# Kernel tuning notes

Measured on AMD Instinct MI355X. Metric: run time of the kernel, lower is better.

## Reference

```python
import jax, jax.numpy as jnp
import numpy as np
from jax import lax

WBITS = 4
BN_EPS = 1e-5


def quantize_weight_symmetric(w, wbits=WBITS):
    # Per-tensor symmetric uniform quantization with straight-through estimator.
    qmax = float(2 ** (wbits - 1) - 1)  # 7 for 4-bit
    scale = jnp.max(jnp.abs(w)) / qmax
    wq = jnp.clip(jnp.round(w / scale), -qmax, qmax) * scale
    # STE: forward uses wq, backward passes gradient straight through to w
    return w + lax.stop_gradient(wq - w)


def setup_inputs() -> dict:
    key = jax.random.key(0)
    k1, k2 = jax.random.split(key)
    x = jax.random.normal(k1, (32, 128, 56, 56), dtype=jnp.float32)
    w = jax.random.normal(k2, (256, 128, 3, 3), dtype=jnp.float32) * 0.05
    gamma = jnp.ones((256,), dtype=jnp.float32)
    beta = jnp.zeros((256,), dtype=jnp.float32)
    return {"x": x, "w": w, "gamma": gamma, "beta": beta}


def reference(x, w, gamma, beta):
    # Quantized conv (QConv, bias=False, stride=1, padding=1)
    wq = quantize_weight_symmetric(w)
    out = lax.conv_general_dilated(
        x, wq,
        window_strides=(1, 1),
        padding=[(1, 1), (1, 1)],
        dimension_numbers=("NCHW", "OIHW", "NCHW"),
    )  # [N, 256, 56, 56]
    # BatchNorm2d in training mode: batch statistics over (N, H, W)
    mean = jnp.mean(out, axis=(0, 2, 3))
    var = jnp.var(out, axis=(0, 2, 3))
    inv = gamma * lax.rsqrt(var + BN_EPS)
    out = out * inv[None, :, None, None] + (beta - mean * inv)[None, :, None, None]
    # abits=32 -> full-precision activation (ReLU)
    return jax.nn.relu(out)
```

## Files before the change

kernel.cpp:

```cpp
#include <hip/hip_runtime.h>

typedef unsigned short u16;
typedef unsigned int u32;
typedef __attribute__((ext_vector_type(4))) float f32x4;
typedef __attribute__((ext_vector_type(8))) short short8;

#define HWD 56
#define HW2 3136
#define C_IN 128
#define K_OUT 256
#define N_IMG 32
#define CHW_IN 401408
#define CHW_OUT 802816
#define PIX 100352
#define WQ_N 294912
#define GROWS 1872
#define XROW 1856
#define XPLANE (GROWS * XROW)
#define NR 12
#define BCHUNKS 2784
#define NSLICE 1568
#define CV_OFF 33554432u
#define WS_NEED_BF16 (CV_OFF + (size_t)PIX * K_OUT * 2)

__device__ __forceinline__ u16 f2bf(float f) {
    u32 u = __float_as_uint(f);
    u32 r = u + 0x7FFFu + ((u >> 16) & 1u);
    return (u16)(r >> 16);
}

__device__ __forceinline__ void glds16(const u16* g, u16* l) {
    __builtin_amdgcn_global_load_lds(
        (const __attribute__((address_space(1))) void*)g,
        (__attribute__((address_space(3))) void*)l, 16, 0, 0);
}

__global__ void maxabs_k(const float* __restrict__ w, u32* __restrict__ wsmax) {
    float m = 0.f;
    for (int i = blockIdx.x * blockDim.x + threadIdx.x; i < WQ_N; i += gridDim.x * blockDim.x)
        m = fmaxf(m, fabsf(w[i]));
    for (int off = 32; off; off >>= 1)
        m = fmaxf(m, __shfl_xor(m, off));
    __shared__ float sm[4];
    int lane = threadIdx.x & 63, wid = threadIdx.x >> 6;
    if (lane == 0) sm[wid] = m;
    __syncthreads();
    if (threadIdx.x == 0) {
        float mm = fmaxf(fmaxf(sm[0], sm[1]), fmaxf(sm[2], sm[3]));
        atomicMax(wsmax, __float_as_uint(mm));
    }
}

__global__ void quant_t_k4(const float* __restrict__ w, const u32* __restrict__ wsmax,
                           u16* __restrict__ wqt4) {
    int o = blockIdx.x * 256 + threadIdx.x;
    if (o >= WQ_N) return;
    int j = o & 7;
    int m = (o >> 3) & 255;
    int oct = (o >> 11) & 3;
    int kt = o >> 13;
    int cq = kt / 9, tap = kt - cq * 9;
    int c = cq * 32 + oct * 8 + j;
    float scale = __uint_as_float(wsmax[0]) / 7.0f;
    float q = rintf(w[(m * 128 + c) * 9 + tap] / scale);
    q = fminf(fmaxf(q, -7.0f), 7.0f);
    wqt4[o] = f2bf(q * scale);
}

__global__ void halo_zero(u16* __restrict__ xt3) {
    int i = blockIdx.x * 256 + threadIdx.x;
    u32 addr;
    if (i < 74240) {
        int rowIdx = i / 928, rem = i - rowIdx * 928;
        int cq = rem / 232, c = rem - cq * 232;
        int row = rowIdx < 64 ? (rowIdx >> 1) * 58 + (rowIdx & 1) * 57 : 1856 + (rowIdx - 64);
        addr = (u32)cq * XPLANE + row * XROW + c * 8;
    } else {
        int j = i - 74240;
        int rowd = j >> 5, rem = j & 31;
        int side = rem >> 4, cq = (rem >> 2) & 3, o4 = rem & 3;
        int n = rowd / 56, h = rowd - n * 56;
        int row = n * 58 + 1 + h, col = side * 57;
        addr = (u32)cq * XPLANE + (row * 58 + col) * 32 + o4 * 8;
    }
    *(uint4*)(xt3 + addr) = (uint4){0, 0, 0, 0};
}

__global__ __launch_bounds__(256) void pad_transpose(const float* __restrict__ x,
                                                     u16* __restrict__ xt3) {
    __shared__ float T[128][57];
    const int tid = threadIdx.x;
    const int n = blockIdx.x / HWD;
    const int h = blockIdx.x - n * HWD;
    const float* srow = x + (size_t)n * CHW_IN + h * HWD;
    #pragma unroll
    for (int it = 0; it < 7; ++it) {
        int i = tid + it * 256;
        int c = i / 14, q = i - c * 14;
        float4 v = *(const float4*)(srow + c * HW2 + q * 4);
        T[c][q * 4 + 0] = v.x; T[c][q * 4 + 1] = v.y;
        T[c][q * 4 + 2] = v.z; T[c][q * 4 + 3] = v.w;
    }
    __syncthreads();
    const int gRow = n * 58 + 1 + h;
    #pragma unroll
    for (int it = 0; it < 4; ++it) {
        int i = tid + it * 256;
        if (i < 56 * 16) {
            int w = i >> 4, oc = i & 15;
            int cq = oc >> 2, o4 = oc & 3;
            union { u16 us[8]; uint4 v4; } pk;
            #pragma unroll
            for (int j = 0; j < 8; ++j) pk.us[j] = f2bf(T[oc * 8 + j][w]);
            *(uint4*)(xt3 + (size_t)cq * XPLANE + (gRow * 58 + (w + 1)) * 32 + o4 * 8) = pk.v4;
        }
    }
}

template <bool BF16OUT>
__global__ __launch_bounds__(512, 2) void conv_m(const u16* __restrict__ xt3,
                                                 const u16* __restrict__ wqt4,
                                                 float* __restrict__ out,
                                                 u16* __restrict__ cvout,
                                                 float* __restrict__ P) {
    __shared__ __align__(16) u16 lds[52416];
    const int tid = threadIdx.x;
    const int lane = tid & 63;
    const int w8 = tid >> 6;
    const int wm = w8 >> 2, wn = w8 & 3;
    const int fr = lane & 15, fq = lane >> 4;
    const int nt = (blockIdx.x & 7) * 49 + (blockIdx.x >> 3);
    const int p0 = nt * 256;
    const int R0 = (p0 / HW2) * 58 + (p0 % HW2) / HWD;

    int bElem[4];
    #pragma unroll
    for (int ni = 0; ni < 4; ++ni) {
        int px = p0 + wn * 64 + ni * 16 + fr;
        int img = px / HW2, hw = px - img * HW2;
        int gr = img * 58 + 1 + hw / HWD;
        int pixLin = (gr - R0) * 58 + (hw % HWD) + 1;
        bElem[ni] = (pixLin - 59) * 40 + fq * 8;
    }
    const int aBase = 27840 + fq * 2048 + (wm * 128 + fr) * 8;

#define GATE2() asm volatile("s_waitcnt vmcnt(2)" ::: "memory")
#define GATE0() asm volatile("s_waitcnt vmcnt(0)" ::: "memory")
#define BAR() __builtin_amdgcn_s_barrier()

    f32x4 acc[8][4];
    #pragma unroll
    for (int a = 0; a < 8; ++a)
        #pragma unroll
        for (int b = 0; b < 4; ++b)
            acc[a][b] = (f32x4){0.f, 0.f, 0.f, 0.f};

    #pragma unroll 1
    for (int cq = 0; cq < 4; ++cq) {
        {
            const u16* bsrc = xt3 + (size_t)cq * XPLANE + (size_t)R0 * XROW;
            uint4 breg[6];
            #pragma unroll
            for (int i = 0; i < 6; ++i) {
                int c = tid + i * 512;
                if (c < BCHUNKS) breg[i] = *(const uint4*)(bsrc + c * 8);
            }
            if (cq == 0) {
                glds16(wqt4 + tid * 8,              &lds[27840 + tid * 8]);
                glds16(wqt4 + (tid + 512) * 8,      &lds[27840 + (tid + 512) * 8]);
                glds16(wqt4 + 8192 + tid * 8,       &lds[27840 + 8192 + tid * 8]);
                glds16(wqt4 + 8192 + (tid + 512) * 8, &lds[27840 + 8192 + (tid + 512) * 8]);
            }
            #pragma unroll
            for (int i = 0; i < 6; ++i) {
                int c = tid + i * 512;
                if (c < BCHUNKS)
                    *(uint4*)&lds[(c >> 2) * 40 + (c & 3) * 8] = breg[i];
            }
        }
        __syncthreads();

        #pragma unroll
        for (int it = 0; it < 3; ++it) {
            #pragma unroll
            for (int u = 0; u < 3; ++u) {
                const int kt = cq * 9 + it * 3 + u;
                if (kt + 2 < 36) {
                    const u16* ga = wqt4 + (kt + 2) * 8192;
                    u16* da = &lds[27840 + ((u + 2) % 3) * 8192];
                    glds16(ga + tid * 8, da + tid * 8);
                    glds16(ga + (tid + 512) * 8, da + (tid + 512) * 8);
                }
                short8 pf[4], wf[4];
                #pragma unroll
                for (int ni = 0; ni < 4; ++ni)
                    pf[ni] = *(const short8*)&lds[bElem[ni] + it * 2320 + u * 40];
                #pragma unroll
                for (int mi = 0; mi < 4; ++mi)
                    wf[mi] = *(const short8*)&lds[aBase + u * 8192 + mi * 128];
                __builtin_amdgcn_s_setprio(1);
                #pragma unroll
                for (int mi = 0; mi < 4; ++mi)
                    #pragma unroll
                    for (int ni = 0; ni < 4; ++ni)
                        acc[mi][ni] = __builtin_amdgcn_mfma_f32_16x16x32_bf16(
                            pf[ni], wf[mi], acc[mi][ni], 0, 0, 0);
                __builtin_amdgcn_s_setprio(0);
                #pragma unroll
                for (int mi = 0; mi < 4; ++mi)
                    wf[mi] = *(const short8*)&lds[aBase + u * 8192 + (mi + 4) * 128];
                __builtin_amdgcn_s_setprio(1);
                #pragma unroll
                for (int mi = 0; mi < 4; ++mi)
                    #pragma unroll
                    for (int ni = 0; ni < 4; ++ni)
                        acc[mi + 4][ni] = __builtin_amdgcn_mfma_f32_16x16x32_bf16(
                            pf[ni], wf[mi], acc[mi + 4][ni], 0, 0, 0);
                __builtin_amdgcn_s_setprio(0);
                if (kt < 34) GATE2();
                else if (kt == 34) GATE0();
                BAR();
            }
        }
    }

    const int slice = nt * 4 + wn;
    #pragma unroll
    for (int mi = 0; mi < 8; ++mi) {
        float s = 0.f, q = 0.f;
        #pragma unroll
        for (int ni = 0; ni < 4; ++ni)
            #pragma unroll
            for (int j = 0; j < 4; ++j) {
                float v = acc[mi][ni][j];
                s += v; q += v * v;
            }
        s += __shfl_xor(s, 16); s += __shfl_xor(s, 32);
        q += __shfl_xor(q, 16); q += __shfl_xor(q, 32);
        if (fq == 0) {
            int ch = wm * 128 + mi * 16 + fr;
            float* dst = P + ((size_t)ch * NSLICE + slice) * 2;
            dst[0] = s; dst[1] = q;
        }
    }

    if (BF16OUT) {
        u16* T = lds;
        #pragma unroll
        for (int p = 0; p < 2; ++p) {
            __syncthreads();
            #pragma unroll
            for (int c2 = 0; c2 < 4; ++c2) {
                const int lch = wm * 64 + c2 * 16 + fr;
                #pragma unroll
                for (int ni = 0; ni < 4; ++ni) {
                    union { u16 h[4]; uint2 v; } pk;
                    #pragma unroll
                    for (int j = 0; j < 4; ++j) pk.h[j] = f2bf(acc[p * 4 + c2][ni][j]);
                    *(uint2*)&T[lch * 264 + wn * 64 + ni * 16 + fq * 4] = pk.v;
                }
            }
            __syncthreads();
            #pragma unroll
            for (int i = 0; i < 8; ++i) {
                int chunk = tid + i * 512;
                int lch = chunk >> 5, pxc = chunk & 31;
                uint4 v = *(const uint4*)&T[lch * 264 + pxc * 8];
                int ch = (lch >> 6) * 128 + p * 64 + (lch & 63);
                *(uint4*)&cvout[(size_t)ch * PIX + p0 + pxc * 8] = v;
            }
        }
    } else {
        #pragma unroll
        for (int mi = 0; mi < 8; ++mi) {
            int ch = wm * 128 + mi * 16 + fr;
            #pragma unroll
            for (int ni = 0; ni < 4; ++ni)
                #pragma unroll
                for (int j = 0; j < 4; ++j) {
                    int px = p0 + wn * 64 + ni * 16 + fq * 4 + j;
                    int n = px / HW2, hw = px - n * HW2;
                    out[(size_t)n * CHW_OUT + (size_t)ch * HW2 + hw] = acc[mi][ni][j];
                }
        }
    }
#undef GATE2
#undef GATE0
#undef BAR
}

__global__ void stats_fin(const float* __restrict__ P, const float* __restrict__ gamma,
                          const float* __restrict__ beta, float* __restrict__ stats) {
    int ch = blockIdx.x;
    int tid = threadIdx.x;
    float s = 0.f, q = 0.f;
    const float* base = P + (size_t)ch * NSLICE * 2;
    for (int i = tid; i < NSLICE; i += 256) {
        float2 v = *(const float2*)(base + i * 2);
        s += v.x; q += v.y;
    }
    for (int m = 32; m; m >>= 1) { s += __shfl_xor(s, m); q += __shfl_xor(q, m); }
    __shared__ float ss[4], qs[4];
    int l = tid & 63, w = tid >> 6;
    if (l == 0) { ss[w] = s; qs[w] = q; }
    __syncthreads();
    if (tid == 0) {
        float S = ss[0] + ss[1] + ss[2] + ss[3];
        float Q = qs[0] + qs[1] + qs[2] + qs[3];
        float mean = S / (float)PIX;
        float var = Q / (float)PIX - mean * mean;
        float inv = gamma[ch] * rsqrtf(var + 1e-5f);
        stats[2 * ch] = inv;
        stats[2 * ch + 1] = beta[ch] - mean * inv;
    }
}

__global__ void bn_relu_nchw(const u16* __restrict__ cvout, float* __restrict__ out,
                             const float* __restrict__ stats) {
    const int b = blockIdx.x;
    const int ch = b / 49, g = b - ch * 49;
    const float inv = stats[2 * ch], sh = stats[2 * ch + 1];
    const int p8 = (g * 256 + threadIdx.x) * 8;
    short8 v = *(const short8*)&cvout[(size_t)ch * PIX + p8];
    const int n = p8 / HW2;
    const int hw = p8 - n * HW2;
    float* dst = out + ((size_t)n * K_OUT + ch) * HW2 + hw;
    f32x4 o0, o1;
    #pragma unroll
    for (int j = 0; j < 4; ++j) {
        float a = __uint_as_float(((u32)(u16)v[j]) << 16);
        float bb = __uint_as_float(((u32)(u16)v[j + 4]) << 16);
        o0[j] = fmaxf(a * inv + sh, 0.f);
        o1[j] = fmaxf(bb * inv + sh, 0.f);
    }
    *(f32x4*)dst = o0;
    *(f32x4*)(dst + 4) = o1;
}

__global__ void bn_relu_f32(float* __restrict__ out, const float* __restrict__ stats) {
    const int n4 = ((size_t)N_IMG * K_OUT * HW2) / 4;
    int stride = gridDim.x * blockDim.x;
    for (int i = blockIdx.x * blockDim.x + threadIdx.x; i < n4; i += stride) {
        int ch = (i / (HW2 / 4)) & (K_OUT - 1);
        float inv = stats[2 * ch], sh = stats[2 * ch + 1];
        f32x4 v = ((f32x4*)out)[i];
        #pragma unroll
        for (int j = 0; j < 4; ++j)
            v[j] = fmaxf(v[j] * inv + sh, 0.f);
        ((f32x4*)out)[i] = v;
    }
}

extern "C" void kernel_launch(void* const* d_in, const int* in_sizes, int n_in,
                              void* d_out, int out_size, void* d_ws, size_t ws_size,
                              hipStream_t stream) {
    const float* x = (const float*)d_in[0];
    const float* w = (const float*)d_in[1];
    const float* gamma = (const float*)d_in[2];
    const float* beta = (const float*)d_in[3];
    float* out = (float*)d_out;

    char* ws = (char*)d_ws;
    u32* wsmax = (u32*)ws;
    float* stats = (float*)(ws + 64);
    u16* wqt4 = (u16*)(ws + 4096);
    float* P = (float*)(ws + 1048576u);
    u16* xt3 = (u16*)(ws + 4325376u);
    u16* cvout = (u16*)(ws + CV_OFF);
    const bool bf16path = (ws_size >= WS_NEED_BF16);

    hipMemsetAsync(wsmax, 0, 64, stream);
    maxabs_k<<<128, 256, 0, stream>>>(w, wsmax);
    quant_t_k4<<<WQ_N / 256, 256, 0, stream>>>(w, wsmax, wqt4);
    halo_zero<<<514, 256, 0, stream>>>(xt3);
    pad_transpose<<<N_IMG * HWD, 256, 0, stream>>>(x, xt3);
    if (bf16path) {
        conv_m<true><<<392, 512, 0, stream>>>(xt3, wqt4, out, cvout, P);
        stats_fin<<<K_OUT, 256, 0, stream>>>(P, gamma, beta, stats);
        bn_relu_nchw<<<K_OUT * 49, 256, 0, stream>>>(cvout, out, stats);
    } else {
        conv_m<false><<<392, 512, 0, stream>>>(xt3, wqt4, out, cvout, P);
        stats_fin<<<K_OUT, 256, 0, stream>>>(P, gamma, beta, stats);
        bn_relu_f32<<<4096, 256, 0, stream>>>(out, stats);
    }
}
```

Before: 150.3 us.

## Split conv output channels across two 256-thread blocks per pixel tile

Each 512-thread block used to compute all 256 output channels for a 256-pixel tile. Now 784 blocks of 256 threads each compute one 128-channel half, with the weight layout rearranged so each half is contiguous. The input tile in LDS is trimmed to 10 rows and weight staging starts before the loop. This shrinks LDS per block to allow more resident blocks and finer scheduling, at the cost of loading each input tile twice across the two halves.

```diff
diff --git a/kernel.cpp b/kernel.cpp
--- a/kernel.cpp
+++ b/kernel.cpp
@@ -17,8 +17,10 @@
 #define GROWS 1872
 #define XROW 1856
 #define XPLANE (GROWS * XROW)
-#define NR 12
-#define BCHUNKS 2784
+#define NR 10
+#define BCHUNKS 2320
+#define BPITCH 40
+#define BELEMS 23200
 #define NSLICE 1568
 #define CV_OFF 33554432u
 #define WS_NEED_BF16 (CV_OFF + (size_t)PIX * K_OUT * 2)
@@ -51,20 +53,22 @@
     }
 }
 
-__global__ void quant_t_k4(const float* __restrict__ w, const u32* __restrict__ wsmax,
-                           u16* __restrict__ wqt4) {
+__global__ void quant_t_k5(const float* __restrict__ w, const u32* __restrict__ wsmax,
+                           u16* __restrict__ wqt) {
     int o = blockIdx.x * 256 + threadIdx.x;
     if (o >= WQ_N) return;
     int j = o & 7;
-    int m = (o >> 3) & 255;
-    int oct = (o >> 11) & 3;
+    int mrow = (o >> 3) & 127;
+    int oct = (o >> 10) & 3;
+    int mt = (o >> 12) & 1;
     int kt = o >> 13;
     int cq = kt / 9, tap = kt - cq * 9;
     int c = cq * 32 + oct * 8 + j;
+    int m = mt * 128 + mrow;
     float scale = __uint_as_float(wsmax[0]) / 7.0f;
     float q = rintf(w[(m * 128 + c) * 9 + tap] / scale);
     q = fminf(fmaxf(q, -7.0f), 7.0f);
-    wqt4[o] = f2bf(q * scale);
+    wqt[o] = f2bf(q * scale);
 }
 
 __global__ void halo_zero(u16* __restrict__ xt3) {
@@ -118,32 +122,37 @@
 }
 
 template <bool BF16OUT>
-__global__ __launch_bounds__(512, 2) void conv_m(const u16* __restrict__ xt3,
-                                                 const u16* __restrict__ wqt4,
+__global__ __launch_bounds__(256, 2) void conv_m(const u16* __restrict__ xt3,
+                                                 const u16* __restrict__ wqt,
                                                  float* __restrict__ out,
                                                  u16* __restrict__ cvout,
                                                  float* __restrict__ P) {
-    __shared__ __align__(16) u16 lds[52416];
+    __shared__ __align__(16) u16 lds[35488];
     const int tid = threadIdx.x;
     const int lane = tid & 63;
-    const int w8 = tid >> 6;
-    const int wm = w8 >> 2, wn = w8 & 3;
+    const int w4 = tid >> 6;
     const int fr = lane & 15, fq = lane >> 4;
-    const int nt = (blockIdx.x & 7) * 49 + (blockIdx.x >> 3);
+    const int swz = (blockIdx.x & 7) * 98 + (blockIdx.x >> 3);
+    const int nt = swz >> 1, mt = swz & 1;
     const int p0 = nt * 256;
     const int R0 = (p0 / HW2) * 58 + (p0 % HW2) / HWD;
 
     int bElem[4];
     #pragma unroll
     for (int ni = 0; ni < 4; ++ni) {
-        int px = p0 + wn * 64 + ni * 16 + fr;
+        int px = p0 + w4 * 64 + ni * 16 + fr;
         int img = px / HW2, hw = px - img * HW2;
         int gr = img * 58 + 1 + hw / HWD;
         int pixLin = (gr - R0) * 58 + (hw % HWD) + 1;
-        bElem[ni] = (pixLin - 59) * 40 + fq * 8;
-    }
-    const int aBase = 27840 + fq * 2048 + (wm * 128 + fr) * 8;
-
+        bElem[ni] = (pixLin - 59) * BPITCH + fq * 8;
+    }
+
+#define ABUF(b) (&lds[BELEMS + (b) * 4096])
+#define STAGE_A(kt_, b_) do {                                              \
+        const u16* ga_ = wqt + (size_t)(((kt_) * 2 + mt)) * 4096;          \
+        glds16(ga_ + tid * 8,         ABUF(b_) + tid * 8);                 \
+        glds16(ga_ + (tid + 256) * 8, ABUF(b_) + (tid + 256) * 8);         \
+    } while (0)
 #define GATE2() asm volatile("s_waitcnt vmcnt(2)" ::: "memory")
 #define GATE0() asm volatile("s_waitcnt vmcnt(0)" ::: "memory")
 #define BAR() __builtin_amdgcn_s_barrier()
@@ -154,28 +163,26 @@
         #pragma unroll
         for (int b = 0; b < 4; ++b)
             acc[a][b] = (f32x4){0.f, 0.f, 0.f, 0.f};
+
+    STAGE_A(0, 0);
+    STAGE_A(1, 1);
 
     #pragma unroll 1
     for (int cq = 0; cq < 4; ++cq) {
         {
             const u16* bsrc = xt3 + (size_t)cq * XPLANE + (size_t)R0 * XROW;
-            uint4 breg[6];
-            #pragma unroll
-            for (int i = 0; i < 6; ++i) {
-                int c = tid + i * 512;
+            uint4 breg[10];
+            #pragma unroll
+            for (int i = 0; i < 10; ++i) {
+                int c = tid + i * 256;
                 if (c < BCHUNKS) breg[i] = *(const uint4*)(bsrc + c * 8);
             }
-            if (cq == 0) {
-                glds16(wqt4 + tid * 8,              &lds[27840 + tid * 8]);
-                glds16(wqt4 + (tid + 512) * 8,      &lds[27840 + (tid + 512) * 8]);
-                glds16(wqt4 + 8192 + tid * 8,       &lds[27840 + 8192 + tid * 8]);
-                glds16(wqt4 + 8192 + (tid + 512) * 8, &lds[27840 + 8192 + (tid + 512) * 8]);
-            }
-            #pragma unroll
-            for (int i = 0; i < 6; ++i) {
-                int c = tid + i * 512;
+            GATE0();
+            #pragma unroll
+            for (int i = 0; i < 10; ++i) {
+                int c = tid + i * 256;
                 if (c < BCHUNKS)
-                    *(uint4*)&lds[(c >> 2) * 40 + (c & 3) * 8] = breg[i];
+                    *(uint4*)&lds[(c >> 2) * BPITCH + (c & 3) * 8] = breg[i];
             }
         }
         __syncthreads();
@@ -184,20 +191,16 @@
         for (int it = 0; it < 3; ++it) {
             #pragma unroll
             for (int u = 0; u < 3; ++u) {
-                const int kt = cq * 9 + it * 3 + u;
-                if (kt + 2 < 36) {
-                    const u16* ga = wqt4 + (kt + 2) * 8192;
-                    u16* da = &lds[27840 + ((u + 2) % 3) * 8192];
-                    glds16(ga + tid * 8, da + tid * 8);
-                    glds16(ga + (tid + 512) * 8, da + (tid + 512) * 8);
-                }
+                const int tt = it * 3 + u;
+                const int kt = cq * 9 + tt;
+                if (kt + 2 < 36) STAGE_A(kt + 2, (tt + 2) % 3);
                 short8 pf[4], wf[4];
                 #pragma unroll
                 for (int ni = 0; ni < 4; ++ni)
-                    pf[ni] = *(const short8*)&lds[bElem[ni] + it * 2320 + u * 40];
+                    pf[ni] = *(const short8*)&lds[bElem[ni] + (it * 58 + u) * BPITCH];
                 #pragma unroll
                 for (int mi = 0; mi < 4; ++mi)
-                    wf[mi] = *(const short8*)&lds[aBase + u * 8192 + mi * 128];
+                    wf[mi] = *(const short8*)&(ABUF(tt % 3)[fq * 1024 + mi * 128 + fr * 8]);
                 __builtin_amdgcn_s_setprio(1);
                 #pragma unroll
                 for (int mi = 0; mi < 4; ++mi)
@@ -208,7 +211,7 @@
                 __builtin_amdgcn_s_setprio(0);
                 #pragma unroll
                 for (int mi = 0; mi < 4; ++mi)
-                    wf[mi] = *(const short8*)&lds[aBase + u * 8192 + (mi + 4) * 128];
+                    wf[mi] = *(const short8*)&(ABUF(tt % 3)[fq * 1024 + (mi + 4) * 128 + fr * 8]);
                 __builtin_amdgcn_s_setprio(1);
                 #pragma unroll
                 for (int mi = 0; mi < 4; ++mi)
@@ -224,7 +227,7 @@
         }
     }
 
-    const int slice = nt * 4 + wn;
+    const int slice = nt * 4 + w4;
     #pragma unroll
     for (int mi = 0; mi < 8; ++mi) {
         float s = 0.f, q = 0.f;
@@ -238,7 +241,7 @@
         s += __shfl_xor(s, 16); s += __shfl_xor(s, 32);
         q += __shfl_xor(q, 16); q += __shfl_xor(q, 32);
         if (fq == 0) {
-            int ch = wm * 128 + mi * 16 + fr;
+            int ch = mt * 128 + mi * 16 + fr;
             float* dst = P + ((size_t)ch * NSLICE + slice) * 2;
             dst[0] = s; dst[1] = q;
         }
@@ -251,39 +254,41 @@
             __syncthreads();
             #pragma unroll
             for (int c2 = 0; c2 < 4; ++c2) {
-                const int lch = wm * 64 + c2 * 16 + fr;
+                const int lch = c2 * 16 + fr;
                 #pragma unroll
                 for (int ni = 0; ni < 4; ++ni) {
                     union { u16 h[4]; uint2 v; } pk;
                     #pragma unroll
                     for (int j = 0; j < 4; ++j) pk.h[j] = f2bf(acc[p * 4 + c2][ni][j]);
-                    *(uint2*)&T[lch * 264 + wn * 64 + ni * 16 + fq * 4] = pk.v;
+                    *(uint2*)&T[lch * 264 + w4 * 64 + ni * 16 + fq * 4] = pk.v;
                 }
             }
             __syncthreads();
             #pragma unroll
             for (int i = 0; i < 8; ++i) {
-                int chunk = tid + i * 512;
-                int lch = chunk >> 5, pxc = chunk & 31;
+                int q = tid + i * 256;
+                int lch = q >> 5, pxc = q & 31;
                 uint4 v = *(const uint4*)&T[lch * 264 + pxc * 8];
-                int ch = (lch >> 6) * 128 + p * 64 + (lch & 63);
+                int ch = mt * 128 + p * 64 + lch;
                 *(uint4*)&cvout[(size_t)ch * PIX + p0 + pxc * 8] = v;
             }
         }
     } else {
         #pragma unroll
         for (int mi = 0; mi < 8; ++mi) {
-            int ch = wm * 128 + mi * 16 + fr;
+            int ch = mt * 128 + mi * 16 + fr;
             #pragma unroll
             for (int ni = 0; ni < 4; ++ni)
                 #pragma unroll
                 for (int j = 0; j < 4; ++j) {
-                    int px = p0 + wn * 64 + ni * 16 + fq * 4 + j;
+                    int px = p0 + w4 * 64 + ni * 16 + fq * 4 + j;
                     int n = px / HW2, hw = px - n * HW2;
                     out[(size_t)n * CHW_OUT + (size_t)ch * HW2 + hw] = acc[mi][ni][j];
                 }
         }
     }
+#undef ABUF
+#undef STAGE_A
 #undef GATE2
 #undef GATE0
 #undef BAR
@@ -363,7 +368,7 @@
     char* ws = (char*)d_ws;
     u32* wsmax = (u32*)ws;
     float* stats = (float*)(ws + 64);
-    u16* wqt4 = (u16*)(ws + 4096);
+    u16* wqt = (u16*)(ws + 4096);
     float* P = (float*)(ws + 1048576u);
     u16* xt3 = (u16*)(ws + 4325376u);
     u16* cvout = (u16*)(ws + CV_OFF);
@@ -371,15 +376,15 @@
 
     hipMemsetAsync(wsmax, 0, 64, stream);
     maxabs_k<<<128, 256, 0, stream>>>(w, wsmax);
-    quant_t_k4<<<WQ_N / 256, 256, 0, stream>>>(w, wsmax, wqt4);
+    quant_t_k5<<<WQ_N / 256, 256, 0, stream>>>(w, wsmax, wqt);
     halo_zero<<<514, 256, 0, stream>>>(xt3);
     pad_transpose<<<N_IMG * HWD, 256, 0, stream>>>(x, xt3);
     if (bf16path) {
-        conv_m<true><<<392, 512, 0, stream>>>(xt3, wqt4, out, cvout, P);
+        conv_m<true><<<784, 256, 0, stream>>>(xt3, wqt, out, cvout, P);
         stats_fin<<<K_OUT, 256, 0, stream>>>(P, gamma, beta, stats);
         bn_relu_nchw<<<K_OUT * 49, 256, 0, stream>>>(cvout, out, stats);
     } else {
-        conv_m<false><<<392, 512, 0, stream>>>(xt3, wqt4, out, cvout, P);
+        conv_m<false><<<784, 256, 0, stream>>>(xt3, wqt, out, cvout, P);
         stats_fin<<<K_OUT, 256, 0, stream>>>(P, gamma, beta, stats);
         bn_relu_f32<<<4096, 256, 0, stream>>>(out, stats);
     }
```

Result: faster. 146.3 us (-2.7%).
